# Performance work log

Hardware: AMD Instinct MI355X
Metric: run time of the kernel (lower is better)

Reference implementation:

```python
import jax, jax.numpy as jnp
import numpy as np

B, L, C_IN = 32, 8192, 64
K, F = 3, 128


def setup_inputs() -> dict:
    key = jax.random.key(0)
    k1, k2 = jax.random.split(key)
    x = jax.random.normal(k1, (B, L, C_IN), dtype=jnp.float32)
    # glorot-ish scale for the conv kernel [k, C_in, F] (TF WIO layout)
    w = jax.random.normal(k2, (K, C_IN, F), dtype=jnp.float32) * (2.0 / (K * C_IN + F)) ** 0.5
    b = jnp.zeros((F,), dtype=jnp.float32)
    return {"x": x, "w": w, "b": b}


def reference(x, w, b):
    # Original: per-position matmul+trace == valid conv1d; then bias + relu.
    # x: [B, L, C_in], w: [K, C_in, F] -> out: [B, L-K+1, F]
    out = jax.lax.conv_general_dilated(
        x, w,
        window_strides=(1,),
        padding="VALID",
        dimension_numbers=("NWC", "WIO", "NWC"),
    )
    return jax.nn.relu(out + b)
```

## Files before the change

kernel.cpp:

```cpp
#include <hip/hip_runtime.h>

typedef __attribute__((ext_vector_type(8))) short short8;
typedef __attribute__((ext_vector_type(4))) float floatx4;

#define B_SZ   32
#define L_IN   8192
#define C_INCH 64
#define KW     3
#define F_OUT  128
#define L_OUT  (L_IN - KW + 1)
#define KDIM   (KW * C_INCH)

#define TILE_L  64
#define AROWS   (TILE_L + 2)
#define ASTRIDE 72

__device__ __forceinline__ short f2bf(float f) {
    unsigned u = __builtin_bit_cast(unsigned, f);
    unsigned r = (u + 0x7fffu + ((u >> 16) & 1u)) >> 16;
    return (short)r;
}

__global__ __launch_bounds__(256, 3) void conv1d_mfma(const float* __restrict__ x,
                                                      const float* __restrict__ w,
                                                      const float* __restrict__ bias,
                                                      float* __restrict__ out) {
    __shared__ short a_lds[AROWS * ASTRIDE];

    const int tid  = threadIdx.x;
    const int b    = blockIdx.y;
    const int l0   = blockIdx.x * TILE_L;
    const int lane = tid & 63;
    const int wave = tid >> 6;
    const int q    = lane >> 4;
    const int nl   = lane & 15;

    short8 bfrag[6][2];
#pragma unroll
    for (int n = 0; n < 2; ++n) {
        const int f = (wave * 2 + n) * 16 + nl;
        const float* __restrict__ wf = w + f;
#pragma unroll
        for (int s = 0; s < 6; ++s) {
            float t[8];
#pragma unroll
            for (int j = 0; j < 8; ++j)
                t[j] = wf[(s * 32 + q * 8 + j) * F_OUT];
            short8 h;
#pragma unroll
            for (int j = 0; j < 8; ++j) h[j] = f2bf(t[j]);
            bfrag[s][n] = h;
        }
    }

#pragma unroll
    for (int i = 0; i < 3; ++i) {
        int c = tid + 256 * i;
        if (c < AROWS * 8) {
            int p   = c >> 3;
            int col = (c & 7) * 8;
            int gl  = l0 + p;
            float4 v0, v1;
            if (gl < L_IN) {
                const float4* xp =
                    (const float4*)(x + ((size_t)b * L_IN + gl) * C_INCH + col);
                v0 = xp[0];
                v1 = xp[1];
            } else {
                v0 = make_float4(0.f, 0.f, 0.f, 0.f);
                v1 = v0;
            }
            short8 h;
            h[0] = f2bf(v0.x); h[1] = f2bf(v0.y); h[2] = f2bf(v0.z); h[3] = f2bf(v0.w);
            h[4] = f2bf(v1.x); h[5] = f2bf(v1.y); h[6] = f2bf(v1.z); h[7] = f2bf(v1.w);
            *(short8*)&a_lds[p * ASTRIDE + col] = h;
        }
    }

    __syncthreads();

    floatx4 acc[4][2];
#pragma unroll
    for (int m = 0; m < 4; ++m)
#pragma unroll
        for (int n = 0; n < 2; ++n) acc[m][n] = (floatx4){0.f, 0.f, 0.f, 0.f};

#pragma unroll
    for (int s = 0; s < 6; ++s) {
        short8 af[4];
#pragma unroll
        for (int m = 0; m < 4; ++m)
            af[m] = *(const short8*)&a_lds[(m * 16 + nl + (s >> 1)) * ASTRIDE
                                           + (s & 1) * 32 + q * 8];
#pragma unroll
        for (int m = 0; m < 4; ++m)
#pragma unroll
            for (int n = 0; n < 2; ++n)
                acc[m][n] = __builtin_amdgcn_mfma_f32_16x16x32_bf16(
                    af[m], bfrag[s][n], acc[m][n], 0, 0, 0);
    }

#pragma unroll
    for (int n = 0; n < 2; ++n) {
        const int f  = (wave * 2 + n) * 16 + nl;
        const float bv = bias[f];
#pragma unroll
        for (int m = 0; m < 4; ++m) {
            const int lb = l0 + m * 16 + q * 4;
#pragma unroll
            for (int r = 0; r < 4; ++r) {
                int l = lb + r;
                if (l < L_OUT) {
                    float v = acc[m][n][r] + bv;
                    out[((size_t)b * L_OUT + l) * F_OUT + f] = v > 0.f ? v : 0.f;
                }
            }
        }
    }
}

extern "C" void kernel_launch(void* const* d_in, const int* in_sizes, int n_in,
                              void* d_out, int out_size, void* d_ws, size_t ws_size,
                              hipStream_t stream) {
    const float* x    = (const float*)d_in[0];
    const float* w    = (const float*)d_in[1];
    const float* bias = (const float*)d_in[2];
    float* out        = (float*)d_out;
    (void)d_ws; (void)ws_size;

    conv1d_mfma<<<dim3(L_IN / TILE_L, B_SZ), 256, 0, stream>>>(x, w, bias, out);
}
```

Before: 221.8 us.

## Prefetch x tile before weight loads, use packed bf16 conversion, raise occupancy

Issues the global loads for the input tile into registers before the weight loads. The bf16 conversion and LDS stores are then interleaved with the weight fragment conversion, so the memory latency of both streams overlaps. It replaces the manual rounding with the packed float2-to-bf162 intrinsic, raises the launch-bounds occupancy hint from 3 to 4, and loads A fragments one at a time next to their MFMAs. Holding the prefetched x values in registers adds register pressure, which conflicts with the higher occupancy target and could cause spills.

```diff
diff --git a/kernel.cpp b/kernel.cpp
--- a/kernel.cpp
+++ b/kernel.cpp
@@ -1,4 +1,5 @@
 #include <hip/hip_runtime.h>
+#include <hip/hip_bf16.h>
 
 typedef __attribute__((ext_vector_type(8))) short short8;
 typedef __attribute__((ext_vector_type(4))) float floatx4;
@@ -15,13 +16,14 @@
 #define AROWS   (TILE_L + 2)
 #define ASTRIDE 72
 
-__device__ __forceinline__ short f2bf(float f) {
-    unsigned u = __builtin_bit_cast(unsigned, f);
-    unsigned r = (u + 0x7fffu + ((u >> 16) & 1u)) >> 16;
-    return (short)r;
+__device__ __forceinline__ unsigned pk2(float a, float b) {
+    __hip_bfloat162 h = __float22bfloat162_rn(make_float2(a, b));
+    unsigned u;
+    __builtin_memcpy(&u, &h, 4);
+    return u;
 }
 
-__global__ __launch_bounds__(256, 3) void conv1d_mfma(const float* __restrict__ x,
+__global__ __launch_bounds__(256, 4) void conv1d_mfma(const float* __restrict__ x,
                                                       const float* __restrict__ w,
                                                       const float* __restrict__ bias,
                                                       float* __restrict__ out) {
@@ -35,6 +37,26 @@
     const int q    = lane >> 4;
     const int nl   = lane & 15;
 
+    float4 xv0[3], xv1[3];
+#pragma unroll
+    for (int i = 0; i < 3; ++i) {
+        int c = tid + 256 * i;
+        if (c < AROWS * 8) {
+            int p   = c >> 3;
+            int col = (c & 7) * 8;
+            int gl  = l0 + p;
+            if (gl < L_IN) {
+                const float4* xp =
+                    (const float4*)(x + ((size_t)b * L_IN + gl) * C_INCH + col);
+                xv0[i] = xp[0];
+                xv1[i] = xp[1];
+            } else {
+                xv0[i] = make_float4(0.f, 0.f, 0.f, 0.f);
+                xv1[i] = xv0[i];
+            }
+        }
+    }
+
     short8 bfrag[6][2];
 #pragma unroll
     for (int n = 0; n < 2; ++n) {
@@ -46,34 +68,28 @@
 #pragma unroll
             for (int j = 0; j < 8; ++j)
                 t[j] = wf[(s * 32 + q * 8 + j) * F_OUT];
-            short8 h;
-#pragma unroll
-            for (int j = 0; j < 8; ++j) h[j] = f2bf(t[j]);
-            bfrag[s][n] = h;
-        }
-    }
 
-#pragma unroll
-    for (int i = 0; i < 3; ++i) {
-        int c = tid + 256 * i;
-        if (c < AROWS * 8) {
-            int p   = c >> 3;
-            int col = (c & 7) * 8;
-            int gl  = l0 + p;
-            float4 v0, v1;
-            if (gl < L_IN) {
-                const float4* xp =
-                    (const float4*)(x + ((size_t)b * L_IN + gl) * C_INCH + col);
-                v0 = xp[0];
-                v1 = xp[1];
-            } else {
-                v0 = make_float4(0.f, 0.f, 0.f, 0.f);
-                v1 = v0;
+            const int bi = n * 6 + s;
+            if (bi < 3) {
+                int c = tid + 256 * bi;
+                if (c < AROWS * 8) {
+                    int p   = c >> 3;
+                    int col = (c & 7) * 8;
+                    union { unsigned u[4]; short8 v; } h;
+                    h.u[0] = pk2(xv0[bi].x, xv0[bi].y);
+                    h.u[1] = pk2(xv0[bi].z, xv0[bi].w);
+                    h.u[2] = pk2(xv1[bi].x, xv1[bi].y);
+                    h.u[3] = pk2(xv1[bi].z, xv1[bi].w);
+                    *(short8*)&a_lds[p * ASTRIDE + col] = h.v;
+                }
             }
-            short8 h;
-            h[0] = f2bf(v0.x); h[1] = f2bf(v0.y); h[2] = f2bf(v0.z); h[3] = f2bf(v0.w);
-            h[4] = f2bf(v1.x); h[5] = f2bf(v1.y); h[6] = f2bf(v1.z); h[7] = f2bf(v1.w);
-            *(short8*)&a_lds[p * ASTRIDE + col] = h;
+
+            union { unsigned u[4]; short8 v; } hb;
+            hb.u[0] = pk2(t[0], t[1]);
+            hb.u[1] = pk2(t[2], t[3]);
+            hb.u[2] = pk2(t[4], t[5]);
+            hb.u[3] = pk2(t[6], t[7]);
+            bfrag[s][n] = hb.v;
         }
     }
 
@@ -87,17 +103,15 @@
 
 #pragma unroll
     for (int s = 0; s < 6; ++s) {
-        short8 af[4];
 #pragma unroll
-        for (int m = 0; m < 4; ++m)
-            af[m] = *(const short8*)&a_lds[(m * 16 + nl + (s >> 1)) * ASTRIDE
-                                           + (s & 1) * 32 + q * 8];
-#pragma unroll
-        for (int m = 0; m < 4; ++m)
+        for (int m = 0; m < 4; ++m) {
+            short8 af = *(const short8*)&a_lds[(m * 16 + nl + (s >> 1)) * ASTRIDE
+                                               + (s & 1) * 32 + q * 8];
 #pragma unroll
             for (int n = 0; n < 2; ++n)
                 acc[m][n] = __builtin_amdgcn_mfma_f32_16x16x32_bf16(
-                    af[m], bfrag[s][n], acc[m][n], 0, 0, 0);
+                    af, bfrag[s][n], acc[m][n], 0, 0, 0);
+        }
     }
 
 #pragma unroll
```

Result: slower. 275.0 us (+24.0%).
